# Kernel tuning notes

Hardware: AMD Instinct MI355X
Metric: run time of the kernel (lower is better)

Reference implementation:

```python
import jax, jax.numpy as jnp
import numpy as np

L, N, E = 2048, 2, 512
H = 8
HD = E // H
FF = 2048
NLAYERS = 2
EPS = 1e-5


def setup_inputs() -> dict:
    key = jax.random.key(0)
    ks = jax.random.split(key, 8)
    s = 0.02
    return {
        "src": jax.random.normal(ks[0], (L, N, E), jnp.float32),
        # packed qkv projection, torch Linear convention: y = x @ W.T + b
        "in_proj_w": jax.random.normal(ks[1], (NLAYERS, 3 * E, E), jnp.float32) * s,
        "in_proj_b": jnp.zeros((NLAYERS, 3 * E), jnp.float32),
        "out_proj_w": jax.random.normal(ks[2], (NLAYERS, E, E), jnp.float32) * s,
        "out_proj_b": jnp.zeros((NLAYERS, E), jnp.float32),
        "lin1_w": jax.random.normal(ks[3], (NLAYERS, FF, E), jnp.float32) * s,
        "lin1_b": jnp.zeros((NLAYERS, FF), jnp.float32),
        "lin2_w": jax.random.normal(ks[4], (NLAYERS, E, FF), jnp.float32) * s,
        "lin2_b": jnp.zeros((NLAYERS, E), jnp.float32),
        "ln1_g": jnp.ones((NLAYERS, E), jnp.float32),
        "ln1_b": jnp.zeros((NLAYERS, E), jnp.float32),
        "ln2_g": jnp.ones((NLAYERS, E), jnp.float32),
        "ln2_b": jnp.zeros((NLAYERS, E), jnp.float32),
    }


def _layer_norm(x, g, b):
    mu = jnp.mean(x, axis=-1, keepdims=True)
    var = jnp.mean(jnp.square(x - mu), axis=-1, keepdims=True)
    return (x - mu) * jax.lax.rsqrt(var + EPS) * g + b


def _mha(x, w_qkv, b_qkv, w_o, b_o):
    # x: [L, N, E] (seq-first, as in torch multi_head_attention_forward)
    qkv = jnp.einsum('lne,fe->lnf', x, w_qkv) + b_qkv  # [L, N, 3E]
    q, k, v = jnp.split(qkv, 3, axis=-1)
    q = q.reshape(L, N, H, HD) * (1.0 / np.sqrt(HD))  # torch scales q pre-bmm
    k = k.reshape(L, N, H, HD)
    v = v.reshape(L, N, H, HD)
    scores = jnp.einsum('lnhd,snhd->nhls', q, k)  # [N, H, L, S] -- O(L*S) matrix
    attn = jax.nn.softmax(scores, axis=-1)
    o = jnp.einsum('nhls,snhd->lnhd', attn, v).reshape(L, N, E)
    return jnp.einsum('lne,fe->lnf', o, w_o) + b_o


def reference(src, in_proj_w, in_proj_b, out_proj_w, out_proj_b,
              lin1_w, lin1_b, lin2_w, lin2_b, ln1_g, ln1_b, ln2_g, ln2_b):
    x = src
    for i in range(NLAYERS):  # fixed small layer count
        a = _mha(x, in_proj_w[i], in_proj_b[i], out_proj_w[i], out_proj_b[i])
        x = _layer_norm(x + a, ln1_g[i], ln1_b[i])  # post-norm (torch default)
        h = jax.nn.relu(jnp.einsum('lne,fe->lnf', x, lin1_w[i]) + lin1_b[i])
        f = jnp.einsum('lnf,ef->lne', h, lin2_w[i]) + lin2_b[i]
        x = _layer_norm(x + f, ln2_g[i], ln2_b[i])
    return x
```

## Files before the change

### kernel.cpp

```cpp
#include <hip/hip_runtime.h>
#include <hip/hip_bf16.h>

using bf16 = __hip_bfloat16;
typedef __bf16 bf16x8 __attribute__((ext_vector_type(8)));
typedef float f32x4 __attribute__((ext_vector_type(4)));

#define MFMA(a, b, c) __builtin_amdgcn_mfma_f32_16x16x32_bf16(a, b, c, 0, 0, 0)

constexpr int L = 2048, N = 2, E = 512, H = 8, HD = 64, FF = 2048;
constexpr int T = L * N;

__global__ void detect_dtype(const unsigned int* __restrict__ g,
                             int* __restrict__ flag) {
  if (threadIdx.x == 0 && blockIdx.x == 0)
    *flag = (g[0] != 0x3F800000u) ? 1 : 0;
}

struct CvtBigArgs {
  const void* src[5];
  bf16* dst[5];
  int n[5];
};
__global__ __launch_bounds__(256) void cvt_big(CvtBigArgs a,
                                               const int* __restrict__ flag) {
  long long idx = (long long)(blockIdx.x * 256 + threadIdx.x) * 8;
  int s = 0;
  while (s < 5 && idx >= a.n[s]) { idx -= a.n[s]; ++s; }
  if (s >= 5) return;
  bf16* dst = a.dst[s];
  if (*flag) {
    *(uint4*)&dst[idx] = *(const uint4*)&((const bf16*)a.src[s])[idx];
  } else {
    const float* src = (const float*)a.src[s];
    float4 x = *(const float4*)&src[idx];
    float4 y = *(const float4*)&src[idx + 4];
    bf16 o8[8] = {__float2bfloat16(x.x), __float2bfloat16(x.y),
                  __float2bfloat16(x.z), __float2bfloat16(x.w),
                  __float2bfloat16(y.x), __float2bfloat16(y.y),
                  __float2bfloat16(y.z), __float2bfloat16(y.w)};
    *(uint4*)&dst[idx] = *(const uint4*)o8;
  }
}

struct CvtParArgs {
  const void* src[8];
  float* dst[8];
  int n[8];
};
__global__ __launch_bounds__(256) void cvt_par(CvtParArgs a,
                                               const int* __restrict__ flag) {
  int idx = blockIdx.x * 256 + threadIdx.x;
  int s = 0;
  while (s < 8 && idx >= a.n[s]) { idx -= a.n[s]; ++s; }
  if (s >= 8) return;
  a.dst[s][idx] = (*flag) ? __bfloat162float(((const bf16*)a.src[s])[idx])
                          : ((const float*)a.src[s])[idx];
}

__device__ __forceinline__ void gload16(const bf16* g, bf16* l) {
  __builtin_amdgcn_global_load_lds(
      (const __attribute__((address_space(1))) unsigned int*)g,
      (__attribute__((address_space(3))) unsigned int*)l, 16, 0, 0);
}

template <bool RELU, int BM, int BN>
__global__ __launch_bounds__(256) void gemm_bt(
    const bf16* __restrict__ A, const bf16* __restrict__ W,
    const float* __restrict__ bias, const bf16* __restrict__ res,
    bf16* __restrict__ C, int M, int F, int K) {
  constexpr int SA = BM / 32;
  constexpr int SB = BN / 32;
  constexpr int MI = BM / 32;
  constexpr int NI = BN / 32;
  __shared__ __align__(16) bf16 As[2][BM * 64];
  __shared__ __align__(16) bf16 Bs[2][BN * 64];
  const int bm = blockIdx.x, bn = blockIdx.y;
  const int tid = threadIdx.x;
  const int w = tid >> 6, lane = tid & 63;
  const int wr = w >> 1, wc = w & 1;
  const int lhi = lane >> 4, llo = lane & 15;
  f32x4 acc[MI][NI] = {};

  const bf16 *ap[SA], *wp[SB];
#pragma unroll
  for (int s = 0; s < SA; ++s) {
    int c = tid + s * 256;
    ap[s] = &A[(size_t)(bm * BM + c % BM) * K + (c / BM) * 8];
  }
#pragma unroll
  for (int s = 0; s < SB; ++s) {
    int c = tid + s * 256;
    wp[s] = &W[(size_t)(bn * BN + c % BN) * K + (c / BN) * 8];
  }
  auto stage = [&](int buf, int k0) {
#pragma unroll
    for (int s = 0; s < SA; ++s)
      gload16(ap[s] + k0, &As[buf][(tid + s * 256) * 8]);
#pragma unroll
    for (int s = 0; s < SB; ++s)
      gload16(wp[s] + k0, &Bs[buf][(tid + s * 256) * 8]);
  };

  stage(0, 0);
  int cur = 0;
  for (int k0 = 0; k0 < K; k0 += 64) {
    __syncthreads();
    if (k0 + 64 < K) stage(cur ^ 1, k0 + 64);
    bf16x8 af[MI][2], bfr[NI][2];
#pragma unroll
    for (int mi = 0; mi < MI; ++mi)
#pragma unroll
      for (int ks = 0; ks < 2; ++ks)
        af[mi][ks] = *(const bf16x8*)&As[cur]
            [((ks * 4 + lhi) * BM + wr * (BM / 2) + mi * 16 + llo) * 8];
#pragma unroll
    for (int ni = 0; ni < NI; ++ni)
#pragma unroll
      for (int ks = 0; ks < 2; ++ks)
        bfr[ni][ks] = *(const bf16x8*)&Bs[cur]
            [((ks * 4 + lhi) * BN + wc * (BN / 2) + ni * 16 + llo) * 8];
    __builtin_amdgcn_s_setprio(1);
#pragma unroll
    for (int ks = 0; ks < 2; ++ks)
#pragma unroll
      for (int mi = 0; mi < MI; ++mi)
#pragma unroll
        for (int ni = 0; ni < NI; ++ni)
          acc[mi][ni] = MFMA(af[mi][ks], bfr[ni][ks], acc[mi][ni]);
    __builtin_amdgcn_s_setprio(0);
    cur ^= 1;
  }
#pragma unroll
  for (int mi = 0; mi < MI; ++mi) {
#pragma unroll
    for (int ni = 0; ni < NI; ++ni) {
      int col = bn * BN + wc * (BN / 2) + ni * 16 + llo;
      float bv = bias[col];
#pragma unroll
      for (int r = 0; r < 4; ++r) {
        int row = bm * BM + wr * (BM / 2) + mi * 16 + lhi * 4 + r;
        float v = acc[mi][ni][r] + bv;
        if (RELU) v = fmaxf(v, 0.f);
        if (res) v += __bfloat162float(res[(size_t)row * F + col]);
        C[(size_t)row * F + col] = __float2bfloat16(v);
      }
    }
  }
}

__global__ __launch_bounds__(256) void prep_kv(
    const bf16* __restrict__ qkv, bf16* __restrict__ kt,
    bf16* __restrict__ vt) {
  __shared__ __align__(16) bf16 Vl[64 * 72];
  const int blk = blockIdx.x;
  const int kb = blk & 31, nh = blk >> 5;
  const int n = nh >> 3, h = nh & 7;
  const int tid = threadIdx.x;
  bf16* ko = kt + ((size_t)nh * 32 + kb) * 4096;
  bf16* vo = vt + ((size_t)nh * 32 + kb) * 4096;
#pragma unroll
  for (int s = 0; s < 2; ++s) {
    int c = tid + s * 256;
    int jj = c >> 3, g = c & 7;
    size_t t = (size_t)((kb * 64 + jj) * N + n);
    uint4 kk = *(const uint4*)&qkv[t * 1536 + 512 + h * 64 + g * 8];
    *(uint4*)&ko[jj * 64 + ((g ^ (jj & 7)) * 8)] = kk;
    uint4 vv = *(const uint4*)&qkv[t * 1536 + 1024 + h * 64 + g * 8];
    *(uint4*)&Vl[jj * 72 + g * 8] = vv;
  }
  __syncthreads();
#pragma unroll
  for (int s = 0; s < 2; ++s) {
    int c = tid + s * 256;
    int d = c >> 3, gsw = c & 7;
    int g = gsw ^ (d & 7);
    bf16 tmp[8];
#pragma unroll
    for (int e = 0; e < 8; ++e) tmp[e] = Vl[(g * 8 + e) * 72 + d];
    *(uint4*)&vo[d * 64 + gsw * 8] = *(const uint4*)tmp;
  }
}

__global__ __launch_bounds__(256) void attn_split(
    const bf16* __restrict__ qkv, const bf16* __restrict__ kt,
    const bf16* __restrict__ vt, bf16* __restrict__ opart,
    float* __restrict__ lpart) {
  __shared__ __align__(16) bf16 Kb[2][4096];
  __shared__ __align__(16) bf16 Vb[2][4096];
  __shared__ __align__(16) bf16 Ps[64 * 72];
  const int blk = blockIdx.x;
  const int rest = blk >> 3;
  const int nh = (blk & 7) * 2 + (rest & 1);
  const int split = (rest >> 1) & 3;
  const int qb = rest >> 3;
  const int n = nh >> 3, h = nh & 7;
  const int tid = threadIdx.x;
  const int w = tid >> 6, lane = tid & 63;
  const int lhi = lane >> 4, llo = lane & 15;
  const int kb0 = split * 8, kb1 = kb0 + 8;

#pragma unroll
  for (int s = 0; s < 2; ++s) {
    int c = tid + s * 256;
    int i = c >> 3, dc = c & 7;
    size_t t = (size_t)((qb * 64 + i) * N + n);
    *(uint4*)&Ps[i * 72 + dc * 8] =
        *(const uint4*)&qkv[t * 1536 + h * 64 + dc * 8];
  }
  __syncthreads();
  bf16x8 aq[2];
  aq[0] = *(const bf16x8*)&Ps[(w * 16 + llo) * 72 + 0 + lhi * 8];
  aq[1] = *(const bf16x8*)&Ps[(w * 16 + llo) * 72 + 32 + lhi * 8];

  const bf16* ktile = kt + (size_t)nh * 32 * 4096;
  const bf16* vtile = vt + (size_t)nh * 32 * 4096;
  auto stage = [&](int buf, int kb) {
#pragma unroll
    for (int s = 0; s < 2; ++s) {
      int c = tid + s * 256;
      gload16(ktile + (size_t)kb * 4096 + c * 8, &Kb[buf][c * 8]);
      gload16(vtile + (size_t)kb * 4096 + c * 8, &Vb[buf][c * 8]);
    }
  };
  stage(0, kb0);

  float psum[4] = {0.f, 0.f, 0.f, 0.f};
  f32x4 o[4] = {};
  int cur = 0;

  for (int kb = kb0; kb < kb1; ++kb) {
    __syncthreads();
    if (kb + 1 < kb1) stage(cur ^ 1, kb + 1);

    f32x4 sfr[4] = {};
    __builtin_amdgcn_s_setprio(1);
#pragma unroll
    for (int cb = 0; cb < 4; ++cb) {
      const int row = cb * 16 + llo;
#pragma unroll
      for (int ks = 0; ks < 2; ++ks) {
        bf16x8 b = *(const bf16x8*)&Kb[cur]
            [row * 64 + (((ks * 4 + lhi) ^ (row & 7)) << 3)];
        sfr[cb] = MFMA(aq[ks], b, sfr[cb]);
      }
    }
    __builtin_amdgcn_s_setprio(0);

#pragma unroll
    for (int cb = 0; cb < 4; ++cb) {
#pragma unroll
      for (int r = 0; r < 4; ++r) {
        float p = __expf(sfr[cb][r] * 0.125f);
        psum[r] += p;
        Ps[(w * 16 + lhi * 4 + r) * 72 + cb * 16 + llo] = __float2bfloat16(p);
      }
    }
    asm volatile("" ::: "memory");

    __builtin_amdgcn_s_setprio(1);
#pragma unroll
    for (int cb = 0; cb < 4; ++cb) {
      const int crow = cb * 16 + llo;
#pragma unroll
      for (int ks = 0; ks < 2; ++ks) {
        bf16x8 a =
            *(const bf16x8*)&Ps[(w * 16 + llo) * 72 + ks * 32 + lhi * 8];
        bf16x8 b = *(const bf16x8*)&Vb[cur]
            [crow * 64 + (((ks * 4 + lhi) ^ (crow & 7)) << 3)];
        o[cb] = MFMA(a, b, o[cb]);
      }
    }
    __builtin_amdgcn_s_setprio(0);
    cur ^= 1;
  }

#pragma unroll
  for (int r = 0; r < 4; ++r) {
    float v = psum[r];
#pragma unroll
    for (int d = 1; d < 16; d <<= 1) v += __shfl_xor(v, d);
    psum[r] = v;
  }
#pragma unroll
  for (int cb = 0; cb < 4; ++cb) {
#pragma unroll
    for (int r = 0; r < 4; ++r) {
      int i = w * 16 + lhi * 4 + r;
      int d = cb * 16 + llo;
      size_t t = (size_t)((qb * 64 + i) * N + n);
      opart[((size_t)split * T + t) * E + h * 64 + d] =
          __float2bfloat16(o[cb][r]);
    }
  }
  if (llo == 0) {
#pragma unroll
    for (int r = 0; r < 4; ++r) {
      int i = w * 16 + lhi * 4 + r;
      size_t t = (size_t)((qb * 64 + i) * N + n);
      lpart[(size_t)(split * T + t) * H + h] = psum[r];
    }
  }
}

__global__ __launch_bounds__(256) void attn_merge(
    const bf16* __restrict__ opart, const float* __restrict__ lpart,
    bf16* __restrict__ atn) {
  int i = (blockIdx.x * 256 + threadIdx.x) * 8;
  if (i >= T * E) return;
  int t = i >> 9, h = (i >> 6) & 7;
  float l = 0.f, acc[8] = {};
#pragma unroll
  for (int s = 0; s < 4; ++s) {
    l += lpart[(size_t)(s * T + t) * H + h];
    uint4 v = *(const uint4*)&opart[(size_t)s * T * E + i];
    const bf16* e8 = (const bf16*)&v;
#pragma unroll
    for (int e = 0; e < 8; ++e) acc[e] += __bfloat162float(e8[e]);
  }
  float rl = 1.f / l;
  bf16 r8[8];
#pragma unroll
  for (int e = 0; e < 8; ++e) r8[e] = __float2bfloat16(acc[e] * rl);
  *(uint4*)&atn[i] = *(const uint4*)r8;
}

template <typename OutT>
__global__ __launch_bounds__(256) void ln_one(
    const bf16* __restrict__ y, const float* __restrict__ g,
    const float* __restrict__ b, OutT* __restrict__ out) {
  const int t = blockIdx.x;
  const int tid = threadIdx.x;
  const int w = tid >> 6, lane = tid & 63;
  const int e = tid * 2;
  const size_t base = (size_t)t * E;
  float v0 = __bfloat162float(y[base + e]);
  float v1 = __bfloat162float(y[base + e + 1]);
  float s = v0 + v1, q = v0 * v0 + v1 * v1;
#pragma unroll
  for (int d = 1; d < 64; d <<= 1) {
    s += __shfl_xor(s, d);
    q += __shfl_xor(q, d);
  }
  __shared__ float rs[4], rq[4];
  if (lane == 0) { rs[w] = s; rq[w] = q; }
  __syncthreads();
  float S = rs[0] + rs[1] + rs[2] + rs[3];
  float Qq = rq[0] + rq[1] + rq[2] + rq[3];
  float mu = S * (1.f / E);
  float var = Qq * (1.f / E) - mu * mu;
  float rstd = rsqrtf(var + 1e-5f);
  float o0 = (v0 - mu) * rstd * g[e] + b[e];
  float o1 = (v1 - mu) * rstd * g[e + 1] + b[e + 1];
  if constexpr (__is_same(OutT, float)) {
    out[base + e] = o0;
    out[base + e + 1] = o1;
  } else {
    out[base + e] = __float2bfloat16(o0);
    out[base + e + 1] = __float2bfloat16(o1);
  }
}

extern "C" void kernel_launch(void* const* d_in, const int* in_sizes, int n_in,
                              void* d_out, int out_size, void* d_ws,
                              size_t ws_size, hipStream_t stream) {
  int* flag = (int*)d_ws;
  float* pbuf = (float*)((char*)d_ws + 16);
  float* in_b = pbuf;
  float* ob   = in_b + 3072;
  float* l1b  = ob + 1024;
  float* l2b  = l1b + 4096;
  float* ln1g = l2b + 1024;
  float* ln1b = ln1g + 1024;
  float* ln2g = ln1b + 1024;
  float* ln2b = ln2g + 1024;
  bf16* big  = (bf16*)(ln2b + 1024);
  bf16* srcb = big;
  bf16* in_w = srcb + (size_t)T * E;
  bf16* ow   = in_w + (size_t)2 * 1536 * E;
  bf16* l1w  = ow + (size_t)2 * E * E;
  bf16* l2w  = l1w + (size_t)2 * FF * E;
  bf16* qkv  = l2w + (size_t)2 * E * FF;
  bf16* atn  = qkv + (size_t)T * 1536;
  bf16* ybuf = atn + (size_t)T * E;
  bf16* x1   = ybuf + (size_t)T * E;
  bf16* x2   = x1 + (size_t)T * E;
  bf16* hbuf = x2 + (size_t)T * E;
  bf16* ktg  = hbuf + (size_t)T * FF;
  bf16* vtg  = ktg + (size_t)T * E;
  bf16* opart  = hbuf;
  float* lpart = (float*)ybuf;

  detect_dtype<<<1, 64, 0, stream>>>((const unsigned int*)d_in[9], flag);
  CvtBigArgs ba;
  ba.src[0] = d_in[0]; ba.dst[0] = srcb; ba.n[0] = T * E;
  ba.src[1] = d_in[1]; ba.dst[1] = in_w; ba.n[1] = 2 * 1536 * E;
  ba.src[2] = d_in[3]; ba.dst[2] = ow;   ba.n[2] = 2 * E * E;
  ba.src[3] = d_in[5]; ba.dst[3] = l1w;  ba.n[3] = 2 * FF * E;
  ba.src[4] = d_in[7]; ba.dst[4] = l2w;  ba.n[4] = 2 * E * FF;
  int btot = ba.n[0] + ba.n[1] + ba.n[2] + ba.n[3] + ba.n[4];
  cvt_big<<<dim3(btot / 2048), 256, 0, stream>>>(ba, flag);
  CvtParArgs pa;
  pa.src[0] = d_in[2];  pa.dst[0] = in_b; pa.n[0] = 3072;
  pa.src[1] = d_in[4];  pa.dst[1] = ob;   pa.n[1] = 1024;
  pa.src[2] = d_in[6];  pa.dst[2] = l1b;  pa.n[2] = 4096;
  pa.src[3] = d_in[8];  pa.dst[3] = l2b;  pa.n[3] = 1024;
  pa.src[4] = d_in[9];  pa.dst[4] = ln1g; pa.n[4] = 1024;
  pa.src[5] = d_in[10]; pa.dst[5] = ln1b; pa.n[5] = 1024;
  pa.src[6] = d_in[11]; pa.dst[6] = ln2g; pa.n[6] = 1024;
  pa.src[7] = d_in[12]; pa.dst[7] = ln2b; pa.n[7] = 1024;
  int ptot = 3072 + 1024 + 4096 + 1024 + 1024 * 4;
  cvt_par<<<dim3(ptot / 256), 256, 0, stream>>>(pa, flag);

  const bf16* x = srcb;
  for (int i = 0; i < 2; ++i) {
    gemm_bt<false, 64, 128><<<dim3(T / 64, 1536 / 128), 256, 0, stream>>>(
        x, in_w + (size_t)i * 1536 * E, in_b + i * 1536, nullptr, qkv,
        T, 1536, E);
    prep_kv<<<dim3(512), 256, 0, stream>>>(qkv, ktg, vtg);
    attn_split<<<dim3(2048), 256, 0, stream>>>(qkv, ktg, vtg, opart, lpart);
    attn_merge<<<dim3(T * E / 2048), 256, 0, stream>>>(opart, lpart, atn);
    gemm_bt<false, 64, 64><<<dim3(T / 64, E / 64), 256, 0, stream>>>(
        atn, ow + (size_t)i * E * E, ob + i * E, x, ybuf, T, E, E);
    ln_one<bf16><<<dim3(T), 256, 0, stream>>>(
        ybuf, ln1g + i * E, ln1b + i * E, x1);
    gemm_bt<true, 64, 128><<<dim3(T / 64, FF / 128), 256, 0, stream>>>(
        x1, l1w + (size_t)i * FF * E, l1b + i * FF, nullptr, hbuf,
        T, FF, E);
    gemm_bt<false, 64, 64><<<dim3(T / 64, E / 64), 256, 0, stream>>>(
        hbuf, l2w + (size_t)i * E * FF, l2b + i * E, x1, ybuf, T, E, FF);
    if (i == 1) {
      ln_one<float><<<dim3(T), 256, 0, stream>>>(
          ybuf, ln2g + i * E, ln2b + i * E, (float*)d_out);
    } else {
      ln_one<bf16><<<dim3(T), 256, 0, stream>>>(
          ybuf, ln2g + i * E, ln2b + i * E, x2);
    }
    x = x2;
  }
}
```

Measured before the change: 354.6 us.

## Double attention query tile per block and enlarge QKV/FFN1 GEMM row tiles

Each attention block now handles 128 query rows instead of 64, with each wave owning two 16-row groups. Every K/V tile staged in shared memory is therefore reused across twice as many queries, and the grid is halved. The QKV and first FFN GEMMs also switch to 128x128 tiles. Fewer blocks and more registers per thread may lower occupancy and wave-level parallelism on the smaller grids.

After: 320.2 us (median of 3 runs). 9.7% less time.

```diff
diff --git a/kernel.cpp b/kernel.cpp
--- a/kernel.cpp
+++ b/kernel.cpp
@@ -187,7 +187,7 @@
     float* __restrict__ lpart) {
   __shared__ __align__(16) bf16 Kb[2][4096];
   __shared__ __align__(16) bf16 Vb[2][4096];
-  __shared__ __align__(16) bf16 Ps[64 * 72];
+  __shared__ __align__(16) bf16 Ps[128 * 72];
   const int blk = blockIdx.x;
   const int rest = blk >> 3;
   const int nh = (blk & 7) * 2 + (rest & 1);
@@ -200,17 +200,21 @@
   const int kb0 = split * 8, kb1 = kb0 + 8;
 
 #pragma unroll
-  for (int s = 0; s < 2; ++s) {
+  for (int s = 0; s < 4; ++s) {
     int c = tid + s * 256;
     int i = c >> 3, dc = c & 7;
-    size_t t = (size_t)((qb * 64 + i) * N + n);
+    size_t t = (size_t)((qb * 128 + i) * N + n);
     *(uint4*)&Ps[i * 72 + dc * 8] =
         *(const uint4*)&qkv[t * 1536 + h * 64 + dc * 8];
   }
   __syncthreads();
-  bf16x8 aq[2];
-  aq[0] = *(const bf16x8*)&Ps[(w * 16 + llo) * 72 + 0 + lhi * 8];
-  aq[1] = *(const bf16x8*)&Ps[(w * 16 + llo) * 72 + 32 + lhi * 8];
+  bf16x8 aq[2][2];
+#pragma unroll
+  for (int rg = 0; rg < 2; ++rg)
+#pragma unroll
+    for (int ks = 0; ks < 2; ++ks)
+      aq[rg][ks] = *(const bf16x8*)
+          &Ps[(w * 32 + rg * 16 + llo) * 72 + ks * 32 + lhi * 8];
 
   const bf16* ktile = kt + (size_t)nh * 32 * 4096;
   const bf16* vtile = vt + (size_t)nh * 32 * 4096;
@@ -224,15 +228,15 @@
   };
   stage(0, kb0);
 
-  float psum[4] = {0.f, 0.f, 0.f, 0.f};
-  f32x4 o[4] = {};
+  float psum[2][4] = {};
+  f32x4 o[2][4] = {};
   int cur = 0;
 
   for (int kb = kb0; kb < kb1; ++kb) {
     __syncthreads();
     if (kb + 1 < kb1) stage(cur ^ 1, kb + 1);
 
-    f32x4 sfr[4] = {};
+    f32x4 sfr[2][4] = {};
     __builtin_amdgcn_s_setprio(1);
 #pragma unroll
     for (int cb = 0; cb < 4; ++cb) {
@@ -241,20 +245,24 @@
       for (int ks = 0; ks < 2; ++ks) {
         bf16x8 b = *(const bf16x8*)&Kb[cur]
             [row * 64 + (((ks * 4 + lhi) ^ (row & 7)) << 3)];
-        sfr[cb] = MFMA(aq[ks], b, sfr[cb]);
+#pragma unroll
+        for (int rg = 0; rg < 2; ++rg)
+          sfr[rg][cb] = MFMA(aq[rg][ks], b, sfr[rg][cb]);
       }
     }
     __builtin_amdgcn_s_setprio(0);
 
 #pragma unroll
-    for (int cb = 0; cb < 4; ++cb) {
-#pragma unroll
-      for (int r = 0; r < 4; ++r) {
-        float p = __expf(sfr[cb][r] * 0.125f);
-        psum[r] += p;
-        Ps[(w * 16 + lhi * 4 + r) * 72 + cb * 16 + llo] = __float2bfloat16(p);
-      }
-    }
+    for (int rg = 0; rg < 2; ++rg)
+#pragma unroll
+      for (int cb = 0; cb < 4; ++cb)
+#pragma unroll
+        for (int r = 0; r < 4; ++r) {
+          float p = __expf(sfr[rg][cb][r] * 0.125f);
+          psum[rg][r] += p;
+          Ps[(w * 32 + rg * 16 + lhi * 4 + r) * 72 + cb * 16 + llo] =
+              __float2bfloat16(p);
+        }
     asm volatile("" ::: "memory");
 
     __builtin_amdgcn_s_setprio(1);
@@ -263,11 +271,14 @@
       const int crow = cb * 16 + llo;
 #pragma unroll
       for (int ks = 0; ks < 2; ++ks) {
-        bf16x8 a =
-            *(const bf16x8*)&Ps[(w * 16 + llo) * 72 + ks * 32 + lhi * 8];
         bf16x8 b = *(const bf16x8*)&Vb[cur]
             [crow * 64 + (((ks * 4 + lhi) ^ (crow & 7)) << 3)];
-        o[cb] = MFMA(a, b, o[cb]);
+#pragma unroll
+        for (int rg = 0; rg < 2; ++rg) {
+          bf16x8 a = *(const bf16x8*)
+              &Ps[(w * 32 + rg * 16 + llo) * 72 + ks * 32 + lhi * 8];
+          o[rg][cb] = MFMA(a, b, o[rg][cb]);
+        }
       }
     }
     __builtin_amdgcn_s_setprio(0);
@@ -275,30 +286,35 @@
   }
 
 #pragma unroll
-  for (int r = 0; r < 4; ++r) {
-    float v = psum[r];
-#pragma unroll
-    for (int d = 1; d < 16; d <<= 1) v += __shfl_xor(v, d);
-    psum[r] = v;
-  }
-#pragma unroll
-  for (int cb = 0; cb < 4; ++cb) {
+  for (int rg = 0; rg < 2; ++rg)
 #pragma unroll
     for (int r = 0; r < 4; ++r) {
-      int i = w * 16 + lhi * 4 + r;
-      int d = cb * 16 + llo;
-      size_t t = (size_t)((qb * 64 + i) * N + n);
-      opart[((size_t)split * T + t) * E + h * 64 + d] =
-          __float2bfloat16(o[cb][r]);
-    }
-  }
+      float v = psum[rg][r];
+#pragma unroll
+      for (int d = 1; d < 16; d <<= 1) v += __shfl_xor(v, d);
+      psum[rg][r] = v;
+    }
+#pragma unroll
+  for (int rg = 0; rg < 2; ++rg)
+#pragma unroll
+    for (int cb = 0; cb < 4; ++cb)
+#pragma unroll
+      for (int r = 0; r < 4; ++r) {
+        int i = w * 32 + rg * 16 + lhi * 4 + r;
+        int d = cb * 16 + llo;
+        size_t t = (size_t)((qb * 128 + i) * N + n);
+        opart[((size_t)split * T + t) * E + h * 64 + d] =
+            __float2bfloat16(o[rg][cb][r]);
+      }
   if (llo == 0) {
 #pragma unroll
-    for (int r = 0; r < 4; ++r) {
-      int i = w * 16 + lhi * 4 + r;
-      size_t t = (size_t)((qb * 64 + i) * N + n);
-      lpart[(size_t)(split * T + t) * H + h] = psum[r];
-    }
+    for (int rg = 0; rg < 2; ++rg)
+#pragma unroll
+      for (int r = 0; r < 4; ++r) {
+        int i = w * 32 + rg * 16 + lhi * 4 + r;
+        size_t t = (size_t)((qb * 128 + i) * N + n);
+        lpart[(size_t)(split * T + t) * H + h] = psum[rg][r];
+      }
   }
 }
 
@@ -413,17 +429,17 @@
 
   const bf16* x = srcb;
   for (int i = 0; i < 2; ++i) {
-    gemm_bt<false, 64, 128><<<dim3(T / 64, 1536 / 128), 256, 0, stream>>>(
+    gemm_bt<false, 128, 128><<<dim3(T / 128, 1536 / 128), 256, 0, stream>>>(
         x, in_w + (size_t)i * 1536 * E, in_b + i * 1536, nullptr, qkv,
         T, 1536, E);
     prep_kv<<<dim3(512), 256, 0, stream>>>(qkv, ktg, vtg);
-    attn_split<<<dim3(2048), 256, 0, stream>>>(qkv, ktg, vtg, opart, lpart);
+    attn_split<<<dim3(1024), 256, 0, stream>>>(qkv, ktg, vtg, opart, lpart);
     attn_merge<<<dim3(T * E / 2048), 256, 0, stream>>>(opart, lpart, atn);
     gemm_bt<false, 64, 64><<<dim3(T / 64, E / 64), 256, 0, stream>>>(
         atn, ow + (size_t)i * E * E, ob + i * E, x, ybuf, T, E, E);
     ln_one<bf16><<<dim3(T), 256, 0, stream>>>(
         ybuf, ln1g + i * E, ln1b + i * E, x1);
-    gemm_bt<true, 64, 128><<<dim3(T / 64, FF / 128), 256, 0, stream>>>(
+    gemm_bt<true, 128, 128><<<dim3(T / 128, FF / 128), 256, 0, stream>>>(
         x1, l1w + (size_t)i * FF * E, l1b + i * FF, nullptr, hbuf,
         T, FF, E);
     gemm_bt<false, 64, 64><<<dim3(T / 64, E / 64), 256, 0, stream>>>(
```
